# Kernel optimization log

Measured on AMD Instinct MI355X. Metric: run time of the kernel, lower is better.

Reference implementation:

```python
import jax, jax.numpy as jnp
import numpy as np

N_NODES = 40000
N_EDGES = 640000
IN, HID, OUT = 128, 256, 47


def setup_inputs() -> dict:
    key = jax.random.key(0)
    ks = jax.random.split(key, 8)
    x = jax.random.normal(ks[0], (N_NODES, IN), dtype=jnp.float32)
    # PyTorch Linear(fan_in, fan_out): store as [fan_in, fan_out] for y = h @ W + b
    W1 = jax.random.normal(ks[1], (2 * IN, HID), dtype=jnp.float32) / np.sqrt(2 * IN)
    b1 = jnp.zeros((HID,), jnp.float32)
    W2 = jax.random.normal(ks[2], (2 * HID, HID), dtype=jnp.float32) / np.sqrt(2 * HID)
    b2 = jnp.zeros((HID,), jnp.float32)
    W3 = jax.random.normal(ks[3], (2 * HID, OUT), dtype=jnp.float32) / np.sqrt(2 * HID)
    b3 = jnp.zeros((OUT,), jnp.float32)
    src = jax.random.randint(ks[4], (N_EDGES,), 0, N_NODES, dtype=jnp.int64 if jax.config.jax_enable_x64 else jnp.int32)
    dst = jax.random.randint(ks[5], (N_EDGES,), 0, N_NODES, dtype=jnp.int64 if jax.config.jax_enable_x64 else jnp.int32)
    return {"x": x, "W1": W1, "b1": b1, "W2": W2, "b2": b2, "W3": W3, "b3": b3,
            "src": src, "dst": dst}


def _sage_layer(h, src, dst, W, b):
    # copy_u -> mean: gather src features, scatter-sum into dst, divide by in-degree
    msum = jax.ops.segment_sum(h[src], dst, num_segments=N_NODES)  # [N, d]
    deg = jax.ops.segment_sum(jnp.ones_like(dst, dtype=h.dtype), dst, num_segments=N_NODES)
    mean = msum / jnp.maximum(deg, 1.0)[:, None]  # zero-degree nodes get 0 (DGL mean convention)
    cat = jnp.concatenate([h, mean], axis=1)      # [N, 2d]
    return cat @ W + b


def reference(x, W1, b1, W2, b2, W3, b3, src, dst):
    # dropout is identity in eval mode
    h = jax.nn.relu(_sage_layer(x, src, dst, W1, b1))
    h = jax.nn.relu(_sage_layer(h, src, dst, W2, b2))
    return _sage_layer(h, src, dst, W3, b3)
```

## Files before the change

### kernel.cpp

```cpp
#include <hip/hip_runtime.h>

#define NNODES 40000
#define NEDGES 640000
#define DIN 128
#define DHID 256
#define DOUT 47
#define NCNT 40960
#define NPART (NCNT / 256)

typedef __attribute__((ext_vector_type(8))) short short8;
typedef __attribute__((ext_vector_type(4))) float f32x4;

__device__ inline float bf2f(unsigned short u) {
    union { unsigned int i; float f; } c; c.i = ((unsigned int)u) << 16; return c.f;
}
__device__ inline unsigned short f2bf(float f) {
    union { float f; unsigned int i; } c; c.f = f;
    unsigned int x = c.i;
    x += 0x7fff + ((x >> 16) & 1);
    return (unsigned short)(x >> 16);
}

__global__ void hist_kernel(const int* __restrict__ dst, int* __restrict__ cnt) {
    int t = blockIdx.x * blockDim.x + threadIdx.x;
    if (t < NEDGES) atomicAdd(&cnt[dst[t]], 1);
}

__global__ void part_kernel(const int* __restrict__ cnt, int* __restrict__ part) {
    int b = blockIdx.x, t = threadIdx.x;
    int v = cnt[b * 256 + t];
#pragma unroll
    for (int off = 32; off > 0; off >>= 1) v += __shfl_down(v, off);
    __shared__ int ws[4];
    if ((t & 63) == 0) ws[t >> 6] = v;
    __syncthreads();
    if (t == 0) part[b] = ws[0] + ws[1] + ws[2] + ws[3];
}

__global__ void scanpart_kernel(const int* __restrict__ part, int* __restrict__ partoff) {
    __shared__ int sh[256];
    int t = threadIdx.x;
    int v = (t < NPART) ? part[t] : 0;
    sh[t] = v;
    __syncthreads();
    for (int off = 1; off < 256; off <<= 1) {
        int add = (t >= off) ? sh[t - off] : 0;
        __syncthreads();
        sh[t] += add;
        __syncthreads();
    }
    if (t < NPART) partoff[t] = sh[t] - v;
}

__global__ void writeptr_kernel(const int* __restrict__ cnt, const int* __restrict__ partoff,
                                int* __restrict__ rowptr) {
    __shared__ int sh[256];
    int b = blockIdx.x, t = threadIdx.x;
    int idx = b * 256 + t;
    int v = cnt[idx];
    sh[t] = v;
    __syncthreads();
    for (int off = 1; off < 256; off <<= 1) {
        int add = (t >= off) ? sh[t - off] : 0;
        __syncthreads();
        sh[t] += add;
        __syncthreads();
    }
    rowptr[idx] = partoff[b] + sh[t] - v;
}

__global__ void fill_kernel(const int* __restrict__ src, const int* __restrict__ dst,
                            const int* __restrict__ rowptr, int* __restrict__ fill,
                            int* __restrict__ eidx) {
    int e = blockIdx.x * blockDim.x + threadIdx.x;
    if (e < NEDGES) {
        int d = dst[e];
        int pos = rowptr[d] + atomicAdd(&fill[d], 1);
        eidx[pos] = src[e];
    }
}

__global__ void f32_to_bf16_kernel(const float* __restrict__ in, unsigned short* __restrict__ out, int n) {
    int t = blockIdx.x * blockDim.x + threadIdx.x;
    if (t < n) out[t] = f2bf(in[t]);
}

__global__ void conv_wt_kernel(const float* __restrict__ W, unsigned short* __restrict__ Wt, int K, int N) {
    int t = blockIdx.x * blockDim.x + threadIdx.x;
    if (t < K * N) {
        int k = t / N, n = t - k * N;
        Wt[(size_t)n * K + k] = f2bf(W[t]);
    }
}

__global__ void conv_wt3_kernel(const float* __restrict__ W3, unsigned short* __restrict__ Wt) {
    int t = blockIdx.x * blockDim.x + threadIdx.x;
    if (t < 94 * 256) {
        int n = t >> 8, k = t & 255;
        float v = (n < 47) ? W3[(size_t)k * DOUT + n]
                           : W3[(size_t)(k + DHID) * DOUT + (n - 47)];
        Wt[t] = f2bf(v);
    }
}

template <int D>
__global__ void agg_bf16_kernel(const unsigned short* __restrict__ h,
                                const int* __restrict__ rowptr,
                                const int* __restrict__ eidx,
                                unsigned short* __restrict__ mean) {
    constexpr int VPL = D / 64;
    const int node = blockIdx.x * (blockDim.x >> 6) + (threadIdx.x >> 6);
    if (node >= NNODES) return;
    const int lane = threadIdx.x & 63;
    const int beg = rowptr[node], end = rowptr[node + 1];
    const unsigned short* hp = h + lane * VPL;

    float acc[VPL];
#pragma unroll
    for (int i = 0; i < VPL; ++i) acc[i] = 0.0f;

    for (int base = beg; base < end; base += 64) {
        int n = min(64, end - base);
        int myidx = (base + lane < end) ? eidx[base + lane] : 0;
        int j = 0;
        for (; j + 4 <= n; j += 4) {
            int s0 = __shfl(myidx, j);
            int s1 = __shfl(myidx, j + 1);
            int s2 = __shfl(myidx, j + 2);
            int s3 = __shfl(myidx, j + 3);
            if constexpr (VPL == 4) {
                ushort4 v0 = *(const ushort4*)(hp + (size_t)s0 * D);
                ushort4 v1 = *(const ushort4*)(hp + (size_t)s1 * D);
                ushort4 v2 = *(const ushort4*)(hp + (size_t)s2 * D);
                ushort4 v3 = *(const ushort4*)(hp + (size_t)s3 * D);
                acc[0] += (bf2f(v0.x) + bf2f(v1.x)) + (bf2f(v2.x) + bf2f(v3.x));
                acc[1] += (bf2f(v0.y) + bf2f(v1.y)) + (bf2f(v2.y) + bf2f(v3.y));
                acc[2] += (bf2f(v0.z) + bf2f(v1.z)) + (bf2f(v2.z) + bf2f(v3.z));
                acc[3] += (bf2f(v0.w) + bf2f(v1.w)) + (bf2f(v2.w) + bf2f(v3.w));
            } else {
                ushort2 v0 = *(const ushort2*)(hp + (size_t)s0 * D);
                ushort2 v1 = *(const ushort2*)(hp + (size_t)s1 * D);
                ushort2 v2 = *(const ushort2*)(hp + (size_t)s2 * D);
                ushort2 v3 = *(const ushort2*)(hp + (size_t)s3 * D);
                acc[0] += (bf2f(v0.x) + bf2f(v1.x)) + (bf2f(v2.x) + bf2f(v3.x));
                acc[1] += (bf2f(v0.y) + bf2f(v1.y)) + (bf2f(v2.y) + bf2f(v3.y));
            }
        }
        for (; j < n; ++j) {
            int s = __shfl(myidx, j);
            if constexpr (VPL == 4) {
                ushort4 v = *(const ushort4*)(hp + (size_t)s * D);
                acc[0] += bf2f(v.x); acc[1] += bf2f(v.y);
                acc[2] += bf2f(v.z); acc[3] += bf2f(v.w);
            } else {
                ushort2 v = *(const ushort2*)(hp + (size_t)s * D);
                acc[0] += bf2f(v.x); acc[1] += bf2f(v.y);
            }
        }
    }
    float inv = (end > beg) ? 1.0f / (float)(end - beg) : 0.0f;
    unsigned short* o = mean + (size_t)node * D + lane * VPL;
    if constexpr (VPL == 4) {
        ushort4 r;
        r.x = f2bf(acc[0] * inv); r.y = f2bf(acc[1] * inv);
        r.z = f2bf(acc[2] * inv); r.w = f2bf(acc[3] * inv);
        *(ushort4*)o = r;
    } else {
        ushort2 r;
        r.x = f2bf(acc[0] * inv); r.y = f2bf(acc[1] * inv);
        *(ushort2*)o = r;
    }
}

__global__ void agg_p_kernel(const unsigned short* __restrict__ P,
                             const int* __restrict__ rowptr,
                             const int* __restrict__ eidx,
                             float* __restrict__ out) {
    const int node = blockIdx.x * (blockDim.x >> 6) + (threadIdx.x >> 6);
    if (node >= NNODES) return;
    const int lane = threadIdx.x & 63;
    const int beg = rowptr[node], end = rowptr[node + 1];
    const bool active = lane < 48;
    const int lc = active ? lane : 0;

    float acc = 0.0f;
    for (int base = beg; base < end; base += 64) {
        int n = min(64, end - base);
        int myidx = (base + lane < end) ? eidx[base + lane] : 0;
        int j = 0;
        for (; j + 4 <= n; j += 4) {
            int s0 = __shfl(myidx, j);
            int s1 = __shfl(myidx, j + 1);
            int s2 = __shfl(myidx, j + 2);
            int s3 = __shfl(myidx, j + 3);
            if (active) {
                float a = bf2f(P[(size_t)s0 * 48 + lc]) + bf2f(P[(size_t)s1 * 48 + lc]);
                float b = bf2f(P[(size_t)s2 * 48 + lc]) + bf2f(P[(size_t)s3 * 48 + lc]);
                acc += a + b;
            }
        }
        for (; j < n; ++j) {
            int s = __shfl(myidx, j);
            if (active) acc += bf2f(P[(size_t)s * 48 + lc]);
        }
    }
    if (lane < 47 && end > beg) {
        out[(size_t)node * DOUT + lane] += acc / (float)(end - beg);
    }
}

template <int MODE>
__launch_bounds__(256, 2)
__global__ void gemm_mfma_kernel(const unsigned short* __restrict__ H,
                                 const unsigned short* __restrict__ Mn,
                                 const unsigned short* __restrict__ Wt,
                                 const float* __restrict__ bias,
                                 void* __restrict__ outp,
                                 unsigned short* __restrict__ Pout,
                                 int d, int N) {
    const int K = 2 * d;
    __shared__ uint4 AsB[128 * 4];
    __shared__ uint4 BsB[128 * 4];

    const int tid = threadIdx.x;
    const int lane = tid & 63;
    const int wid = tid >> 6;
    const int wr = wid >> 1, wc = wid & 1;
    const int row0 = blockIdx.x * 128;
    const int col0 = blockIdx.y * 128;

    const int sr = tid >> 1;
    const int sh = tid & 1;
    const int gar = min(row0 + sr, NNODES - 1);
    const int gbr = min(col0 + sr, N - 1);
    const int ssw = (sr >> 1) & 3;

    f32x4 acc[4][4];
#pragma unroll
    for (int m = 0; m < 4; ++m)
#pragma unroll
        for (int n = 0; n < 4; ++n) {
            f32x4 z = {0.0f, 0.0f, 0.0f, 0.0f};
            acc[m][n] = z;
        }

    for (int k0 = 0; k0 < K; k0 += 32) {
        {
            int kb = k0 + sh * 16;
            const unsigned short* p;
            if (MODE == 2) {
                p = H + (size_t)gar * K + kb;
            } else {
                p = (kb < d) ? (H + (size_t)gar * d + kb)
                             : (Mn + (size_t)gar * d + (kb - d));
            }
            uint4 v0 = *(const uint4*)p;
            uint4 v1 = *(const uint4*)(p + 8);
            AsB[sr * 4 + ((2 * sh) ^ ssw)]     = v0;
            AsB[sr * 4 + ((2 * sh + 1) ^ ssw)] = v1;
        }
        {
            const unsigned short* p = Wt + (size_t)gbr * K + k0 + sh * 16;
            uint4 v0 = *(const uint4*)p;
            uint4 v1 = *(const uint4*)(p + 8);
            BsB[sr * 4 + ((2 * sh) ^ ssw)]     = v0;
            BsB[sr * 4 + ((2 * sh + 1) ^ ssw)] = v1;
        }
        __syncthreads();

        short8 af[4], bfr[4];
        const int fr = lane & 15;
        const int slot = lane >> 4;
#pragma unroll
        for (int m = 0; m < 4; ++m) {
            int r = wr * 64 + m * 16 + fr;
            union { uint4 u; short8 s; } c;
            c.u = AsB[r * 4 + (slot ^ ((r >> 1) & 3))];
            af[m] = c.s;
        }
#pragma unroll
        for (int n = 0; n < 4; ++n) {
            int r = wc * 64 + n * 16 + fr;
            union { uint4 u; short8 s; } c;
            c.u = BsB[r * 4 + (slot ^ ((r >> 1) & 3))];
            bfr[n] = c.s;
        }
#pragma unroll
        for (int m = 0; m < 4; ++m)
#pragma unroll
            for (int n = 0; n < 4; ++n)
                acc[m][n] = __builtin_amdgcn_mfma_f32_16x16x32_bf16(af[m], bfr[n], acc[m][n], 0, 0, 0);
        __syncthreads();
    }

#pragma unroll
    for (int m = 0; m < 4; ++m) {
#pragma unroll
        for (int n = 0; n < 4; ++n) {
            int col = col0 + wc * 64 + n * 16 + (lane & 15);
            if (col >= N) continue;
            float bv = (MODE == 0) ? bias[col] : ((col < 47) ? bias[col] : 0.0f);
#pragma unroll
            for (int q = 0; q < 4; ++q) {
                int row = row0 + wr * 64 + m * 16 + (lane >> 4) * 4 + q;
                if (row < NNODES) {
                    float v = acc[m][n][q] + bv;
                    if (MODE == 0) {
                        v = fmaxf(v, 0.0f);
                        ((unsigned short*)outp)[(size_t)row * N + col] = f2bf(v);
                    } else {
                        if (col < 47) ((float*)outp)[(size_t)row * DOUT + col] = v;
                        else Pout[(size_t)row * 48 + (col - 47)] = f2bf(v);
                    }
                }
            }
        }
    }
}

extern "C" void kernel_launch(void* const* d_in, const int* in_sizes, int n_in,
                              void* d_out, int out_size, void* d_ws, size_t ws_size,
                              hipStream_t stream) {
    const float* x  = (const float*)d_in[0];
    const float* W1 = (const float*)d_in[1];
    const float* b1 = (const float*)d_in[2];
    const float* W2 = (const float*)d_in[3];
    const float* b2 = (const float*)d_in[4];
    const float* W3 = (const float*)d_in[5];
    const float* b3 = (const float*)d_in[6];
    const int* src  = (const int*)d_in[7];
    const int* dst  = (const int*)d_in[8];
    float* out = (float*)d_out;

    int* rowptr  = (int*)d_ws;
    int* eidx    = rowptr + NCNT;
    int* cnt     = eidx + NEDGES;
    int* fill    = cnt + NCNT;
    int* part    = fill + NCNT;
    int* partoff = part + 256;
    unsigned short* xbf  = (unsigned short*)(partoff + 256);
    unsigned short* h1   = xbf + (size_t)NNODES * DIN;
    unsigned short* h2   = h1 + (size_t)NNODES * DHID;
    unsigned short* mean = h2 + (size_t)NNODES * DHID;
    unsigned short* wt1  = mean + (size_t)NNODES * DHID;
    unsigned short* wt2  = wt1 + 2 * DIN * DHID;
    unsigned short* wt3  = wt2 + 2 * DHID * DHID;
    unsigned short* P    = mean;

    hipMemsetAsync(cnt, 0, 2 * NCNT * sizeof(int), stream);
    hist_kernel<<<(NEDGES + 255) / 256, 256, 0, stream>>>(dst, cnt);
    part_kernel<<<NPART, 256, 0, stream>>>(cnt, part);
    scanpart_kernel<<<1, 256, 0, stream>>>(part, partoff);
    writeptr_kernel<<<NPART, 256, 0, stream>>>(cnt, partoff, rowptr);
    fill_kernel<<<(NEDGES + 255) / 256, 256, 0, stream>>>(src, dst, rowptr, fill, eidx);

    f32_to_bf16_kernel<<<(NNODES * DIN + 255) / 256, 256, 0, stream>>>(x, xbf, NNODES * DIN);
    conv_wt_kernel<<<(2 * DIN * DHID + 255) / 256, 256, 0, stream>>>(W1, wt1, 2 * DIN, DHID);
    conv_wt_kernel<<<(2 * DHID * DHID + 255) / 256, 256, 0, stream>>>(W2, wt2, 2 * DHID, DHID);
    conv_wt3_kernel<<<(94 * 256 + 255) / 256, 256, 0, stream>>>(W3, wt3);

    const int MB = (NNODES + 127) / 128;

    agg_bf16_kernel<DIN><<<NNODES / 4, 256, 0, stream>>>(xbf, rowptr, eidx, mean);
    {
        dim3 grid(MB, 2);
        gemm_mfma_kernel<0><<<grid, 256, 0, stream>>>(xbf, mean, wt1, b1, h1, nullptr, DIN, DHID);
    }

    agg_bf16_kernel<DHID><<<NNODES / 4, 256, 0, stream>>>(h1, rowptr, eidx, mean);
    {
        dim3 grid(MB, 2);
        gemm_mfma_kernel<0><<<grid, 256, 0, stream>>>(h1, mean, wt2, b2, h2, nullptr, DHID, DHID);
    }

    {
        dim3 grid(MB, 1);
        gemm_mfma_kernel<2><<<grid, 256, 0, stream>>>(h2, h2, wt3, b3, out, P, DHID / 2, 94);
    }
    agg_p_kernel<<<NNODES / 4, 256, 0, stream>>>(P, rowptr, eidx, out);
}
```

Before: 243.9 us.

## Slice aggregation by feature columns and store edge indices as 16-bit

Replaces the per-node aggregation kernel with a column-sliced one. Each grid x-block covers a 32-feature slice, and each wave splits its lanes into 4 edge sub-groups of 16 lanes. Partial sums are reduced with xor-shuffles. The goal is to keep each pass's working set of gathered rows small enough to stay cache-resident and to expose more memory parallelism. Edge source indices are narrowed to 16-bit to halve index traffic, nontemporal loads and stores are added, and the x-to-bf16 conversion is vectorised. The 16-bit indices are only valid because node ids are below 65536 here. Each slice re-reads the CSR indices, so index traffic grows with the number of slices.

```diff
diff --git a/kernel.cpp b/kernel.cpp
--- a/kernel.cpp
+++ b/kernel.cpp
@@ -71,18 +71,23 @@
 
 __global__ void fill_kernel(const int* __restrict__ src, const int* __restrict__ dst,
                             const int* __restrict__ rowptr, int* __restrict__ fill,
-                            int* __restrict__ eidx) {
+                            unsigned short* __restrict__ eidx) {
     int e = blockIdx.x * blockDim.x + threadIdx.x;
     if (e < NEDGES) {
         int d = dst[e];
         int pos = rowptr[d] + atomicAdd(&fill[d], 1);
-        eidx[pos] = src[e];
-    }
-}
-
-__global__ void f32_to_bf16_kernel(const float* __restrict__ in, unsigned short* __restrict__ out, int n) {
+        eidx[pos] = (unsigned short)src[e];
+    }
+}
+
+__global__ void f32_to_bf16x4_kernel(const float4* __restrict__ in, ushort4* __restrict__ out, int n4) {
     int t = blockIdx.x * blockDim.x + threadIdx.x;
-    if (t < n) out[t] = f2bf(in[t]);
+    if (t < n4) {
+        float4 v = in[t];
+        ushort4 r;
+        r.x = f2bf(v.x); r.y = f2bf(v.y); r.z = f2bf(v.z); r.w = f2bf(v.w);
+        out[t] = r;
+    }
 }
 
 __global__ void conv_wt_kernel(const float* __restrict__ W, unsigned short* __restrict__ Wt, int K, int N) {
@@ -104,77 +109,55 @@
 }
 
 template <int D>
-__global__ void agg_bf16_kernel(const unsigned short* __restrict__ h,
-                                const int* __restrict__ rowptr,
-                                const int* __restrict__ eidx,
-                                unsigned short* __restrict__ mean) {
-    constexpr int VPL = D / 64;
-    const int node = blockIdx.x * (blockDim.x >> 6) + (threadIdx.x >> 6);
+__global__ void agg_sliced_kernel(const unsigned short* __restrict__ h,
+                                  const int* __restrict__ rowptr,
+                                  const unsigned short* __restrict__ eidx,
+                                  unsigned short* __restrict__ mean) {
+    const int c = blockIdx.x;
+    const int node = blockIdx.y * 16 + (threadIdx.x >> 6);
     if (node >= NNODES) return;
     const int lane = threadIdx.x & 63;
-    const int beg = rowptr[node], end = rowptr[node + 1];
-    const unsigned short* hp = h + lane * VPL;
-
-    float acc[VPL];
-#pragma unroll
-    for (int i = 0; i < VPL; ++i) acc[i] = 0.0f;
-
-    for (int base = beg; base < end; base += 64) {
-        int n = min(64, end - base);
-        int myidx = (base + lane < end) ? eidx[base + lane] : 0;
-        int j = 0;
-        for (; j + 4 <= n; j += 4) {
-            int s0 = __shfl(myidx, j);
-            int s1 = __shfl(myidx, j + 1);
-            int s2 = __shfl(myidx, j + 2);
-            int s3 = __shfl(myidx, j + 3);
-            if constexpr (VPL == 4) {
-                ushort4 v0 = *(const ushort4*)(hp + (size_t)s0 * D);
-                ushort4 v1 = *(const ushort4*)(hp + (size_t)s1 * D);
-                ushort4 v2 = *(const ushort4*)(hp + (size_t)s2 * D);
-                ushort4 v3 = *(const ushort4*)(hp + (size_t)s3 * D);
-                acc[0] += (bf2f(v0.x) + bf2f(v1.x)) + (bf2f(v2.x) + bf2f(v3.x));
-                acc[1] += (bf2f(v0.y) + bf2f(v1.y)) + (bf2f(v2.y) + bf2f(v3.y));
-                acc[2] += (bf2f(v0.z) + bf2f(v1.z)) + (bf2f(v2.z) + bf2f(v3.z));
-                acc[3] += (bf2f(v0.w) + bf2f(v1.w)) + (bf2f(v2.w) + bf2f(v3.w));
-            } else {
-                ushort2 v0 = *(const ushort2*)(hp + (size_t)s0 * D);
-                ushort2 v1 = *(const ushort2*)(hp + (size_t)s1 * D);
-                ushort2 v2 = *(const ushort2*)(hp + (size_t)s2 * D);
-                ushort2 v3 = *(const ushort2*)(hp + (size_t)s3 * D);
-                acc[0] += (bf2f(v0.x) + bf2f(v1.x)) + (bf2f(v2.x) + bf2f(v3.x));
-                acc[1] += (bf2f(v0.y) + bf2f(v1.y)) + (bf2f(v2.y) + bf2f(v3.y));
-            }
-        }
-        for (; j < n; ++j) {
-            int s = __shfl(myidx, j);
-            if constexpr (VPL == 4) {
-                ushort4 v = *(const ushort4*)(hp + (size_t)s * D);
-                acc[0] += bf2f(v.x); acc[1] += bf2f(v.y);
-                acc[2] += bf2f(v.z); acc[3] += bf2f(v.w);
-            } else {
-                ushort2 v = *(const ushort2*)(hp + (size_t)s * D);
-                acc[0] += bf2f(v.x); acc[1] += bf2f(v.y);
-            }
-        }
-    }
-    float inv = (end > beg) ? 1.0f / (float)(end - beg) : 0.0f;
-    unsigned short* o = mean + (size_t)node * D + lane * VPL;
-    if constexpr (VPL == 4) {
-        ushort4 r;
-        r.x = f2bf(acc[0] * inv); r.y = f2bf(acc[1] * inv);
-        r.z = f2bf(acc[2] * inv); r.w = f2bf(acc[3] * inv);
-        *(ushort4*)o = r;
-    } else {
-        ushort2 r;
-        r.x = f2bf(acc[0] * inv); r.y = f2bf(acc[1] * inv);
-        *(ushort2*)o = r;
+    const int esub = lane >> 4;
+    const int f2 = lane & 15;
+    const int beg = __builtin_nontemporal_load(rowptr + node);
+    const int end = __builtin_nontemporal_load(rowptr + node + 1);
+    const unsigned short* hp = h + c * 32 + f2 * 2;
+
+    float ax = 0.0f, ay = 0.0f;
+    int j = beg;
+    for (; j + 8 <= end; j += 8) {
+        int s0 = (int)__builtin_nontemporal_load(eidx + j + esub);
+        int s1 = (int)__builtin_nontemporal_load(eidx + j + 4 + esub);
+        ushort2 v0 = *(const ushort2*)(hp + (size_t)s0 * D);
+        ushort2 v1 = *(const ushort2*)(hp + (size_t)s1 * D);
+        ax += bf2f(v0.x) + bf2f(v1.x);
+        ay += bf2f(v0.y) + bf2f(v1.y);
+    }
+    for (; j + 4 <= end; j += 4) {
+        int s0 = (int)__builtin_nontemporal_load(eidx + j + esub);
+        ushort2 v0 = *(const ushort2*)(hp + (size_t)s0 * D);
+        ax += bf2f(v0.x);
+        ay += bf2f(v0.y);
+    }
+    int rem = end - j;
+    if (rem > 0) {
+        int jj = j + (esub < rem ? esub : 0);
+        int s0 = (int)__builtin_nontemporal_load(eidx + jj);
+        ushort2 v0 = *(const ushort2*)(hp + (size_t)s0 * D);
+        if (esub < rem) { ax += bf2f(v0.x); ay += bf2f(v0.y); }
+    }
+    ax += __shfl_xor(ax, 16); ay += __shfl_xor(ay, 16);
+    ax += __shfl_xor(ax, 32); ay += __shfl_xor(ay, 32);
+    if (lane < 16) {
+        float inv = (end > beg) ? 1.0f / (float)(end - beg) : 0.0f;
+        unsigned int rv = (unsigned int)f2bf(ax * inv) | ((unsigned int)f2bf(ay * inv) << 16);
+        __builtin_nontemporal_store(rv, (unsigned int*)(mean + (size_t)node * D + c * 32 + lane * 2));
     }
 }
 
 __global__ void agg_p_kernel(const unsigned short* __restrict__ P,
                              const int* __restrict__ rowptr,
-                             const int* __restrict__ eidx,
+                             const unsigned short* __restrict__ eidx,
                              float* __restrict__ out) {
     const int node = blockIdx.x * (blockDim.x >> 6) + (threadIdx.x >> 6);
     if (node >= NNODES) return;
@@ -186,7 +169,7 @@
     float acc = 0.0f;
     for (int base = beg; base < end; base += 64) {
         int n = min(64, end - base);
-        int myidx = (base + lane < end) ? eidx[base + lane] : 0;
+        int myidx = (base + lane < end) ? (int)__builtin_nontemporal_load(eidx + base + lane) : 0;
         int j = 0;
         for (; j + 4 <= n; j += 4) {
             int s0 = __shfl(myidx, j);
@@ -274,16 +257,16 @@
 #pragma unroll
         for (int m = 0; m < 4; ++m) {
             int r = wr * 64 + m * 16 + fr;
-            union { uint4 u; short8 s; } c;
-            c.u = AsB[r * 4 + (slot ^ ((r >> 1) & 3))];
-            af[m] = c.s;
+            union { uint4 u; short8 s; } cc;
+            cc.u = AsB[r * 4 + (slot ^ ((r >> 1) & 3))];
+            af[m] = cc.s;
         }
 #pragma unroll
         for (int n = 0; n < 4; ++n) {
             int r = wc * 64 + n * 16 + fr;
-            union { uint4 u; short8 s; } c;
-            c.u = BsB[r * 4 + (slot ^ ((r >> 1) & 3))];
-            bfr[n] = c.s;
+            union { uint4 u; short8 s; } cc;
+            cc.u = BsB[r * 4 + (slot ^ ((r >> 1) & 3))];
+            bfr[n] = cc.s;
         }
 #pragma unroll
         for (int m = 0; m < 4; ++m)
@@ -333,8 +316,8 @@
     float* out = (float*)d_out;
 
     int* rowptr  = (int*)d_ws;
-    int* eidx    = rowptr + NCNT;
-    int* cnt     = eidx + NEDGES;
+    unsigned short* eidx = (unsigned short*)(rowptr + NCNT);
+    int* cnt     = (int*)(eidx + NEDGES);
     int* fill    = cnt + NCNT;
     int* part    = fill + NCNT;
     int* partoff = part + 256;
@@ -354,20 +337,28 @@
     writeptr_kernel<<<NPART, 256, 0, stream>>>(cnt, partoff, rowptr);
     fill_kernel<<<(NEDGES + 255) / 256, 256, 0, stream>>>(src, dst, rowptr, fill, eidx);
 
-    f32_to_bf16_kernel<<<(NNODES * DIN + 255) / 256, 256, 0, stream>>>(x, xbf, NNODES * DIN);
+    f32_to_bf16x4_kernel<<<(NNODES * DIN / 4 + 255) / 256, 256, 0, stream>>>(
+        (const float4*)x, (ushort4*)xbf, NNODES * DIN / 4);
     conv_wt_kernel<<<(2 * DIN * DHID + 255) / 256, 256, 0, stream>>>(W1, wt1, 2 * DIN, DHID);
     conv_wt_kernel<<<(2 * DHID * DHID + 255) / 256, 256, 0, stream>>>(W2, wt2, 2 * DHID, DHID);
     conv_wt3_kernel<<<(94 * 256 + 255) / 256, 256, 0, stream>>>(W3, wt3);
 
     const int MB = (NNODES + 127) / 128;
-
-    agg_bf16_kernel<DIN><<<NNODES / 4, 256, 0, stream>>>(xbf, rowptr, eidx, mean);
+    const int NGRP = (NNODES + 15) / 16;
+
+    {
+        dim3 grid(DIN / 32, NGRP);
+        agg_sliced_kernel<DIN><<<grid, 1024, 0, stream>>>(xbf, rowptr, eidx, mean);
+    }
     {
         dim3 grid(MB, 2);
         gemm_mfma_kernel<0><<<grid, 256, 0, stream>>>(xbf, mean, wt1, b1, h1, nullptr, DIN, DHID);
     }
 
-    agg_bf16_kernel<DHID><<<NNODES / 4, 256, 0, stream>>>(h1, rowptr, eidx, mean);
+    {
+        dim3 grid(DHID / 32, NGRP);
+        agg_sliced_kernel<DHID><<<grid, 1024, 0, stream>>>(h1, rowptr, eidx, mean);
+    }
     {
         dim3 grid(MB, 2);
         gemm_mfma_kernel<0><<<grid, 256, 0, stream>>>(h1, mean, wt2, b2, h2, nullptr, DHID, DHID);
```

After: 402.4 us. +65.0%, slower.
